# Optimization experiments

Measured on AMD Instinct MI355X. Metric: run time of the kernel, lower is better.

## Reference

```python
import jax, jax.numpy as jnp
import numpy as np

B, N, NODE_DIM = 8, 128, 64
L, RES_DIM = 512, 1024
CG, CP = 128, 128
NUM_GNN_STEPS = 3
HID = CG + CP // 2  # interaction hidden = 192


def setup_inputs() -> dict:
    key = jax.random.key(0)
    ks = jax.random.split(key, 20)
    a = (jax.random.uniform(ks[0], (B, N, N)) < 0.05).astype(jnp.float32)
    adj = jnp.clip(a + jnp.swapaxes(a, 1, 2), 0.0, 1.0)
    adj = adj * (1.0 - jnp.eye(N, dtype=jnp.float32))
    nodes = jax.random.normal(ks[1], (B, N, NODE_DIM), dtype=jnp.float32)
    prot = jax.random.normal(ks[2], (B, L, RES_DIM), dtype=jnp.float32)
    s = 0.02
    inp = {
        "adj_mats": adj, "nodes": nodes, "protein_sequences": prot,
        "Wn": jax.random.normal(ks[3], (NODE_DIM, CG)) * s, "bn": jnp.zeros((CG,)),
        "Wg": jax.random.normal(ks[4], (CG, CG)) * s, "bg": jnp.zeros((CG,)),
        "Wr": jax.random.normal(ks[5], (RES_DIM, CP)) * s, "br": jnp.zeros((CP,)),
        "Wa": jax.random.normal(ks[6], (CG + CP, 1)) * s, "ba": jnp.zeros((1,)),
        "W1": jax.random.normal(ks[7], (CG + CP, HID)) * s, "b1": jnp.zeros((HID,)),
        "W2": jax.random.normal(ks[8], (HID, CG)) * s, "b2": jnp.zeros((CG,)),
        "Wo": jax.random.normal(ks[9], (CG, 1)) * s, "bo": jnp.zeros((1,)),
    }
    return inp


def reference(adj_mats, nodes, protein_sequences,
              Wn, bn, Wg, bg, Wr, br, Wa, ba, W1, b1, W2, b2, Wo, bo):
    # node compression: [B,N,CG]
    h = nodes @ Wn + bn
    deg = jnp.clip(jnp.sum(adj_mats, axis=-1), 1.0, None)        # [B,N]
    norm = deg ** -0.5                                           # [B,N]
    for i in range(NUM_GNN_STEPS):
        m = jnp.einsum('bij,bjc->bic', adj_mats, h * norm[..., None])
        h = (m * norm[..., None]) @ Wg + bg
        h = jnp.tanh(h) if i == NUM_GNN_STEPS - 1 else jax.nn.relu(h)
    # residue compression: [B,L,CP]
    r = protein_sequences @ Wr + br
    # MergeSnE1: all-pairs broadcast concat -> [B, N*L, CG+CP]
    cat = jnp.concatenate([
        jnp.broadcast_to(h[:, :, None, :], (B, N, L, CG)),
        jnp.broadcast_to(r[:, None, :, :], (B, N, L, CP)),
    ], axis=-1).reshape(B, N * L, CG + CP)
    # attention: Linear -> Softmax over last dim (size 1 => all ones, faithful)
    attn = jax.nn.softmax(cat @ Wa + ba, axis=-1)                # [B,N*L,1]
    inter = jax.nn.relu(cat @ W1 + b1) @ W2 + b2                 # [B,N*L,CG]
    weighted_sum = jnp.sum(attn * inter, axis=1)                 # [B,CG]
    return weighted_sum @ Wo + bo                                # [B,1]
```

## Files before the change

### kernel.cpp

```cpp
#include <hip/hip_runtime.h>

#define BB 8
#define NN 128
#define ND 64
#define LL 512
#define RD 1024
#define CG 128
#define HID 192

typedef __attribute__((ext_vector_type(8))) short short8;
typedef __attribute__((ext_vector_type(4))) float f32x4;

__device__ __forceinline__ unsigned short f2bf(float x) {
    unsigned u = __builtin_bit_cast(unsigned, x);
    u += 0x7fffu + ((u >> 16) & 1u);
    return (unsigned short)(u >> 16);
}
__device__ __forceinline__ float bf2f(unsigned short h) {
    unsigned u = ((unsigned)h) << 16;
    return __builtin_bit_cast(float, u);
}
#define MFMA __builtin_amdgcn_mfma_f32_16x16x32_bf16

__global__ __launch_bounds__(512, 1) void k_prep(
    const float* __restrict__ adj, const float* __restrict__ nodes,
    const float* __restrict__ Wn, const float* __restrict__ bn,
    const float* __restrict__ Wr, const float* __restrict__ br,
    const float* __restrict__ W1, const float* __restrict__ b1,
    const float* __restrict__ Wg, const float* __restrict__ bg,
    const float* __restrict__ W2, const float* __restrict__ b2,
    const float* __restrict__ Wo, const float* __restrict__ bo,
    unsigned short* __restrict__ WcT, unsigned short* __restrict__ hW1b,
    float* __restrict__ vbuf, float* __restrict__ out)
{
    __shared__ unsigned short hT[NN][136];
    __shared__ unsigned short mbuf[NN][72];
    __shared__ unsigned short WgT[NN][136];
    __shared__ unsigned short W1T[HID][136];
    __shared__ float snorm[NN];
    __shared__ float b1cL[HID];
    __shared__ float sbg[NN];
    int t = threadIdx.x, blk = blockIdx.x;
    int w = t >> 6, l = t & 63, lr = l & 15, ks = l >> 4, lk = ks * 8;
    const float* W1b = W1 + CG * HID;

    if (blk < 16) {
        int r0 = blk * 64;
        #pragma unroll
        for (int q = 0; q < 48; ++q) {
            int e = t + 512 * q;
            int m = e / HID, c = e % HID;
            W1T[c][m] = f2bf(W1[(size_t)(CG + m) * HID + c]);
        }
        int rt = w & 3, jh = w >> 2;
        short8 awr[4];
        #pragma unroll
        for (int kk = 0; kk < 4; ++kk) {
            const float* wp = Wr + (size_t)(r0 + rt * 16 + lr) * CG + kk * 32 + lk;
            float4 q0 = *(const float4*)wp;
            float4 q1 = *(const float4*)(wp + 4);
            unsigned short u[8];
            u[0]=f2bf(q0.x); u[1]=f2bf(q0.y); u[2]=f2bf(q0.z); u[3]=f2bf(q0.w);
            u[4]=f2bf(q1.x); u[5]=f2bf(q1.y); u[6]=f2bf(q1.z); u[7]=f2bf(q1.w);
            awr[kk] = *(const short8*)u;
        }
        __syncthreads();
        #pragma unroll
        for (int jt6 = 0; jt6 < 6; ++jt6) {
            int jt = jh * 6 + jt6;
            f32x4 d = {0.f, 0.f, 0.f, 0.f};
            #pragma unroll
            for (int kk = 0; kk < 4; ++kk) {
                short8 bf = *(const short8*)(&W1T[jt * 16 + lr][kk * 32 + lk]);
                d = MFMA(awr[kk], bf, d, 0, 0, 0);
            }
            unsigned short u[4];
            #pragma unroll
            for (int i = 0; i < 4; ++i) u[i] = f2bf(d[i]);
            *(uint2*)(WcT + (size_t)(jt * 16 + lr) * RD + r0 + rt * 16 + ks * 4) = *(uint2*)u;
        }
        return;
    }
    if (blk == 16) {
        if (t < HID) {
            float s = 0.f;
            #pragma unroll 8
            for (int k = 0; k < CG; ++k) s = fmaf(W2[t * CG + k], Wo[k], s);
            vbuf[t] = s;
        }
        if (t < BB) {
            float s = 0.f;
            for (int k = 0; k < CG; ++k) s = fmaf(b2[k], Wo[k], s);
            out[t] = (float)(NN * LL) * s + bo[0];
        }
        return;
    }

    int b = blk - 17;
    int i0 = w * 16;

    {
        float* dscr = (float*)&mbuf[0][0];
        int row = t >> 2, q4 = t & 3;
        const float* ar = adj + ((size_t)b * NN + row) * NN + q4 * 32;
        float d = 0.f;
        #pragma unroll
        for (int c4 = 0; c4 < 8; ++c4) {
            float4 p = *(const float4*)(ar + c4 * 4);
            d += (p.x + p.y) + (p.z + p.w);
        }
        dscr[row * 4 + q4] = d;
        __syncthreads();
        if (t < NN) {
            snorm[t] = rsqrtf(fmaxf(dscr[t*4] + dscr[t*4+1] + dscr[t*4+2] + dscr[t*4+3], 1.f));
        } else if (t < 320) {
            int j = t - 128;
            float s = b1[j];
            #pragma unroll 8
            for (int m = 0; m < CG; ++m)
                s = fmaf(br[m], W1b[(size_t)m * HID + j], s);
            b1cL[j] = s;
        } else if (t < 448) {
            sbg[t - 320] = bg[t - 320];
        }
        __syncthreads();
    }

    unsigned short* WnT = &mbuf[0][0];
    #pragma unroll
    for (int q = 0; q < 16; ++q) {
        int e = t + 512 * q;
        int c = e & 127, k = e >> 7;
        WnT[c * 72 + k] = f2bf(Wn[(size_t)k * CG + c]);
    }
    #pragma unroll
    for (int q = 0; q < 32; ++q) {
        int e = t + 512 * q;
        int c = e & 127, j = e >> 7;
        WgT[c][j] = f2bf(Wg[(size_t)j * CG + c]);
    }
    #pragma unroll
    for (int q = 0; q < 32; ++q) {
        int e = t + 512 * q;
        int jj = e & 127, k = e >> 7;
        W1T[jj][k] = f2bf(W1[(size_t)k * HID + jj]);
    }
    #pragma unroll
    for (int q = 0; q < 16; ++q) {
        int e = t + 512 * q;
        int jj = 128 + (e & 63), k = e >> 6;
        W1T[jj][k] = f2bf(W1[(size_t)k * HID + jj]);
    }

    short8 af[4];
    {
        float ni = snorm[i0 + lr];
        const float* ar = adj + ((size_t)b * NN + i0 + lr) * NN;
        #pragma unroll
        for (int kk = 0; kk < 4; ++kk) {
            int kb = kk * 32 + lk;
            float4 p0 = *(const float4*)(ar + kb);
            float4 p1 = *(const float4*)(ar + kb + 4);
            unsigned short u[8];
            u[0] = f2bf(p0.x * ni * snorm[kb+0]); u[1] = f2bf(p0.y * ni * snorm[kb+1]);
            u[2] = f2bf(p0.z * ni * snorm[kb+2]); u[3] = f2bf(p0.w * ni * snorm[kb+3]);
            u[4] = f2bf(p1.x * ni * snorm[kb+4]); u[5] = f2bf(p1.y * ni * snorm[kb+5]);
            u[6] = f2bf(p1.z * ni * snorm[kb+6]); u[7] = f2bf(p1.w * ni * snorm[kb+7]);
            af[kk] = *(const short8*)u;
        }
    }
    short8 bnod[2];
    #pragma unroll
    for (int kk = 0; kk < 2; ++kk) {
        const float* np = nodes + ((size_t)b * NN + i0 + lr) * ND + kk * 32 + lk;
        float4 q0 = *(const float4*)np;
        float4 q1 = *(const float4*)(np + 4);
        unsigned short u[8];
        u[0]=f2bf(q0.x); u[1]=f2bf(q0.y); u[2]=f2bf(q0.z); u[3]=f2bf(q0.w);
        u[4]=f2bf(q1.x); u[5]=f2bf(q1.y); u[6]=f2bf(q1.z); u[7]=f2bf(q1.w);
        bnod[kk] = *(const short8*)u;
    }
    __syncthreads();

    #pragma unroll
    for (int ct = 0; ct < 8; ++ct) {
        f32x4 d = {0.f, 0.f, 0.f, 0.f};
        #pragma unroll
        for (int kk = 0; kk < 2; ++kk) {
            short8 afw = *(const short8*)(WnT + (ct * 16 + lr) * 72 + kk * 32 + lk);
            d = MFMA(afw, bnod[kk], d, 0, 0, 0);
        }
        #pragma unroll
        for (int i = 0; i < 4; ++i)
            hT[ct * 16 + ks * 4 + i][i0 + lr] = f2bf(d[i] + bn[ct * 16 + ks * 4 + i]);
    }
    __syncthreads();

    for (int s = 0; s < 3; ++s) {
        f32x4 acc8[8];
        #pragma unroll
        for (int ct = 0; ct < 8; ++ct) acc8[ct] = (f32x4){0.f, 0.f, 0.f, 0.f};
        #pragma unroll
        for (int hf = 0; hf < 2; ++hf) {
            #pragma unroll
            for (int jt = 0; jt < 4; ++jt) {
                int jg = hf * 64 + jt * 16;
                f32x4 d = {0.f, 0.f, 0.f, 0.f};
                #pragma unroll
                for (int kk = 0; kk < 4; ++kk) {
                    short8 bf = *(const short8*)(&hT[jg + lr][kk * 32 + lk]);
                    d = MFMA(af[kk], bf, d, 0, 0, 0);
                }
                #pragma unroll
                for (int i = 0; i < 4; ++i)
                    mbuf[i0 + ks * 4 + i][jt * 16 + lr] = f2bf(d[i]);
            }
            short8 bm[2];
            #pragma unroll
            for (int kk = 0; kk < 2; ++kk)
                bm[kk] = *(const short8*)(&mbuf[i0 + lr][kk * 32 + lk]);
            #pragma unroll
            for (int ct = 0; ct < 8; ++ct) {
                #pragma unroll
                for (int kk = 0; kk < 2; ++kk) {
                    short8 wf = *(const short8*)(&WgT[ct * 16 + lr][hf * 64 + kk * 32 + lk]);
                    if (s < 2)
                        acc8[ct] = MFMA(wf, bm[kk], acc8[ct], 0, 0, 0);
                    else
                        acc8[ct] = MFMA(bm[kk], wf, acc8[ct], 0, 0, 0);
                }
            }
        }
        __syncthreads();
        if (s < 2) {
            #pragma unroll
            for (int ct = 0; ct < 8; ++ct)
                #pragma unroll
                for (int i = 0; i < 4; ++i)
                    hT[ct * 16 + ks * 4 + i][i0 + lr] =
                        f2bf(fmaxf(acc8[ct][i] + sbg[ct * 16 + ks * 4 + i], 0.f));
        } else {
            #pragma unroll
            for (int ct = 0; ct < 8; ++ct)
                #pragma unroll
                for (int i = 0; i < 4; ++i)
                    hT[i0 + ks * 4 + i][ct * 16 + lr] =
                        f2bf(tanhf(acc8[ct][i] + sbg[ct * 16 + lr]));
        }
        __syncthreads();
    }

    {
        short8 bh[4];
        #pragma unroll
        for (int kk = 0; kk < 4; ++kk)
            bh[kk] = *(const short8*)(&hT[i0 + lr][kk * 32 + lk]);
        #pragma unroll
        for (int jjt = 0; jjt < 12; ++jjt) {
            f32x4 d = {0.f, 0.f, 0.f, 0.f};
            #pragma unroll
            for (int kk = 0; kk < 4; ++kk) {
                short8 wf = *(const short8*)(&W1T[jjt * 16 + lr][kk * 32 + lk]);
                d = MFMA(wf, bh[kk], d, 0, 0, 0);
            }
            #pragma unroll
            for (int i = 0; i < 4; ++i) {
                int jj = jjt * 16 + ks * 4 + i;
                hW1b[(size_t)b * HID * NN + jj * NN + i0 + lr] = f2bf(d[i] + b1cL[jj]);
            }
        }
    }
}

__global__ __launch_bounds__(512, 1) void k_gemm(
    const float* __restrict__ prot, const unsigned short* __restrict__ WcT,
    const unsigned short* __restrict__ hW1b, const float* __restrict__ vbuf,
    float* __restrict__ out)
{
    __shared__ unsigned short aT[16 * 1032];
    __shared__ unsigned short h1[HID * 136];
    __shared__ float pbuf[2 * 16 * 192];
    __shared__ float sred[8];
    int t = threadIdx.x, blk = blockIdx.x;
    int b = blk >> 5, lc = blk & 31;
    int w = t >> 6, l = t & 63, lr = l & 15, ks = l >> 4, lk = ks * 8;
    int w2 = w >> 2, wj = w & 3;

    #pragma unroll
    for (int q = 0; q < 4; ++q) {
        int e = t + 512 * q;
        int row = e >> 7;
        int c8 = (e & 127) * 8;
        const float* pr = prot + ((size_t)(b * LL + lc * 16 + row)) * RD + c8;
        float4 p0 = *(const float4*)pr;
        float4 p1 = *(const float4*)(pr + 4);
        unsigned short u[8];
        u[0]=f2bf(p0.x); u[1]=f2bf(p0.y); u[2]=f2bf(p0.z); u[3]=f2bf(p0.w);
        u[4]=f2bf(p1.x); u[5]=f2bf(p1.y); u[6]=f2bf(p1.z); u[7]=f2bf(p1.w);
        *(short8*)(aT + row * 1032 + c8) = *(const short8*)u;
    }
    #pragma unroll
    for (int q = 0; q < 6; ++q) {
        int u8 = t + 512 * q;
        int row = u8 >> 4;
        int n8 = (u8 & 15) * 8;
        short8 v = *(const short8*)(hW1b + (size_t)b * HID * NN + row * NN + n8);
        *(short8*)(h1 + row * 136 + n8) = v;
    }
    float v0 = vbuf[wj * 48 + lr];
    float v1 = vbuf[wj * 48 + 16 + lr];
    float v2 = vbuf[wj * 48 + 32 + lr];
    __syncthreads();

    f32x4 a0 = {0.f,0.f,0.f,0.f}, a1 = a0, a2 = a0;
    {
        const unsigned short* ap = aT + lr * 1032 + w2 * 512 + lk;
        const unsigned short* bp = WcT + (size_t)(wj * 48 + lr) * RD + w2 * 512 + lk;
        #pragma unroll 4
        for (int k0 = 0; k0 < 512; k0 += 32) {
            short8 av = *(const short8*)(ap + k0);
            short8 b0 = *(const short8*)(bp + k0);
            short8 b1 = *(const short8*)(bp + 16 * RD + k0);
            short8 b2 = *(const short8*)(bp + 32 * RD + k0);
            a0 = MFMA(av, b0, a0, 0, 0, 0);
            a1 = MFMA(av, b1, a1, 0, 0, 0);
            a2 = MFMA(av, b2, a2, 0, 0, 0);
        }
    }
    #pragma unroll
    for (int i = 0; i < 4; ++i) {
        int r = ks * 4 + i;
        pbuf[(w2 * 16 + r) * 192 + wj * 48 + lr]      = a0[i];
        pbuf[(w2 * 16 + r) * 192 + wj * 48 + 16 + lr] = a1[i];
        pbuf[(w2 * 16 + r) * 192 + wj * 48 + 32 + lr] = a2[i];
    }
    __syncthreads();
    float rw0[4], rw1[4], rw2[4];
    #pragma unroll
    for (int i = 0; i < 4; ++i) {
        int r = ks * 4 + i;
        rw0[i] = pbuf[r * 192 + wj*48 + lr]      + pbuf[(16 + r) * 192 + wj*48 + lr];
        rw1[i] = pbuf[r * 192 + wj*48 + 16 + lr] + pbuf[(16 + r) * 192 + wj*48 + 16 + lr];
        rw2[i] = pbuf[r * 192 + wj*48 + 32 + lr] + pbuf[(16 + r) * 192 + wj*48 + 32 + lr];
    }

    const unsigned short* h0p = h1 + (wj * 48 + lr) * 136 + w2 * 64;
    const unsigned short* h1p = h0p + 16 * 136;
    const unsigned short* h2p = h0p + 32 * 136;
    float s = 0.f;
    #pragma unroll 2
    for (int n0 = 0; n0 < 64; n0 += 4) {
        unsigned short e0[4], e1[4], e2[4];
        *(uint2*)e0 = *(const uint2*)(h0p + n0);
        *(uint2*)e1 = *(const uint2*)(h1p + n0);
        *(uint2*)e2 = *(const uint2*)(h2p + n0);
        #pragma unroll
        for (int q = 0; q < 4; ++q) {
            float hh0 = bf2f(e0[q]), hh1 = bf2f(e1[q]), hh2 = bf2f(e2[q]);
            #pragma unroll
            for (int i = 0; i < 4; ++i) {
                s = fmaf(v0, fmaxf(rw0[i] + hh0, 0.f), s);
                s = fmaf(v1, fmaxf(rw1[i] + hh1, 0.f), s);
                s = fmaf(v2, fmaxf(rw2[i] + hh2, 0.f), s);
            }
        }
    }
    for (int off = 32; off; off >>= 1) s += __shfl_down(s, off);
    if (l == 0) sred[w] = s;
    __syncthreads();
    if (t == 0) {
        float tot = ((sred[0] + sred[1]) + (sred[2] + sred[3]))
                  + ((sred[4] + sred[5]) + (sred[6] + sred[7]));
        atomicAdd(&out[b], tot);
    }
}

extern "C" void kernel_launch(void* const* d_in, const int* in_sizes, int n_in,
                              void* d_out, int out_size, void* d_ws, size_t ws_size,
                              hipStream_t stream)
{
    const float* adj   = (const float*)d_in[0];
    const float* nodes = (const float*)d_in[1];
    const float* prot  = (const float*)d_in[2];
    const float* Wn    = (const float*)d_in[3];
    const float* bn    = (const float*)d_in[4];
    const float* Wg    = (const float*)d_in[5];
    const float* bg    = (const float*)d_in[6];
    const float* Wr    = (const float*)d_in[7];
    const float* br    = (const float*)d_in[8];
    const float* W1    = (const float*)d_in[11];
    const float* b1    = (const float*)d_in[12];
    const float* W2    = (const float*)d_in[13];
    const float* b2    = (const float*)d_in[14];
    const float* Wo    = (const float*)d_in[15];
    const float* bo    = (const float*)d_in[16];

    float* ws     = (float*)d_ws;
    float* vbuf   = ws;
    unsigned short* hW1b = (unsigned short*)(ws + 192);
    unsigned short* WcT  = hW1b + (size_t)BB * HID * NN;
    float* out    = (float*)d_out;

    hipLaunchKernelGGL(k_prep, dim3(25), dim3(512), 0, stream,
                       adj, nodes, Wn, bn, Wr, br, W1, b1, Wg, bg,
                       W2, b2, Wo, bo, WcT, hW1b, vbuf, out);
    hipLaunchKernelGGL(k_gemm, dim3(256), dim3(512), 0, stream,
                       prot, WcT, hW1b, vbuf, out);
}
```

Measured before the change: 55.18 us.

## Vectorize weight transposes, drop h1 LDS staging, split accumulators, raise occupancy

Weight transposes in k_prep now use float4 global loads, each spread over four LDS stores, where before every element needed its own scalar load. k_gemm stops staging hW1b into shared memory and reads it straight from global memory (L2-resident). This frees about 52KB of LDS, and launch bounds are raised to 4 blocks per CU. The epilogue reduction uses four independent accumulators to break the serial FMA dependency chain. Direct global reads in the inner loop may add latency, and the higher launch bound may cap the register count.

Measured after the change: 63.40 us. 1.15x slower.

```diff
diff --git a/kernel.cpp b/kernel.cpp
--- a/kernel.cpp
+++ b/kernel.cpp
@@ -47,10 +47,14 @@
     if (blk < 16) {
         int r0 = blk * 64;
         #pragma unroll
-        for (int q = 0; q < 48; ++q) {
-            int e = t + 512 * q;
-            int m = e / HID, c = e % HID;
-            W1T[c][m] = f2bf(W1[(size_t)(CG + m) * HID + c]);
+        for (int q = 0; q < 12; ++q) {
+            int e4 = t + 512 * q;
+            int m = e4 / 48, c = (e4 % 48) * 4;
+            float4 v = *(const float4*)(W1 + (size_t)(CG + m) * HID + c);
+            W1T[c][m]     = f2bf(v.x);
+            W1T[c + 1][m] = f2bf(v.y);
+            W1T[c + 2][m] = f2bf(v.z);
+            W1T[c + 3][m] = f2bf(v.w);
         }
         int rt = w & 3, jh = w >> 2;
         short8 awr[4];
@@ -128,28 +132,34 @@
 
     unsigned short* WnT = &mbuf[0][0];
     #pragma unroll
-    for (int q = 0; q < 16; ++q) {
-        int e = t + 512 * q;
-        int c = e & 127, k = e >> 7;
-        WnT[c * 72 + k] = f2bf(Wn[(size_t)k * CG + c]);
-    }
-    #pragma unroll
-    for (int q = 0; q < 32; ++q) {
-        int e = t + 512 * q;
-        int c = e & 127, j = e >> 7;
-        WgT[c][j] = f2bf(Wg[(size_t)j * CG + c]);
-    }
-    #pragma unroll
-    for (int q = 0; q < 32; ++q) {
-        int e = t + 512 * q;
-        int jj = e & 127, k = e >> 7;
-        W1T[jj][k] = f2bf(W1[(size_t)k * HID + jj]);
-    }
-    #pragma unroll
-    for (int q = 0; q < 16; ++q) {
-        int e = t + 512 * q;
-        int jj = 128 + (e & 63), k = e >> 6;
-        W1T[jj][k] = f2bf(W1[(size_t)k * HID + jj]);
+    for (int q = 0; q < 4; ++q) {
+        int e4 = t + 512 * q;
+        int k = e4 >> 5, c = (e4 & 31) * 4;
+        float4 v = *(const float4*)(Wn + (size_t)k * CG + c);
+        WnT[c * 72 + k]       = f2bf(v.x);
+        WnT[(c + 1) * 72 + k] = f2bf(v.y);
+        WnT[(c + 2) * 72 + k] = f2bf(v.z);
+        WnT[(c + 3) * 72 + k] = f2bf(v.w);
+    }
+    #pragma unroll
+    for (int q = 0; q < 8; ++q) {
+        int e4 = t + 512 * q;
+        int j = e4 >> 5, c = (e4 & 31) * 4;
+        float4 v = *(const float4*)(Wg + (size_t)j * CG + c);
+        WgT[c][j]     = f2bf(v.x);
+        WgT[c + 1][j] = f2bf(v.y);
+        WgT[c + 2][j] = f2bf(v.z);
+        WgT[c + 3][j] = f2bf(v.w);
+    }
+    #pragma unroll
+    for (int q = 0; q < 12; ++q) {
+        int e4 = t + 512 * q;
+        int k = e4 / 48, jj = (e4 % 48) * 4;
+        float4 v = *(const float4*)(W1 + (size_t)k * HID + jj);
+        W1T[jj][k]     = f2bf(v.x);
+        W1T[jj + 1][k] = f2bf(v.y);
+        W1T[jj + 2][k] = f2bf(v.z);
+        W1T[jj + 3][k] = f2bf(v.w);
     }
 
     short8 af[4];
@@ -272,13 +282,12 @@
     }
 }
 
-__global__ __launch_bounds__(512, 1) void k_gemm(
+__global__ __launch_bounds__(512, 4) void k_gemm(
     const float* __restrict__ prot, const unsigned short* __restrict__ WcT,
     const unsigned short* __restrict__ hW1b, const float* __restrict__ vbuf,
     float* __restrict__ out)
 {
     __shared__ unsigned short aT[16 * 1032];
-    __shared__ unsigned short h1[HID * 136];
     __shared__ float pbuf[2 * 16 * 192];
     __shared__ float sred[8];
     int t = threadIdx.x, blk = blockIdx.x;
@@ -298,14 +307,6 @@
         u[0]=f2bf(p0.x); u[1]=f2bf(p0.y); u[2]=f2bf(p0.z); u[3]=f2bf(p0.w);
         u[4]=f2bf(p1.x); u[5]=f2bf(p1.y); u[6]=f2bf(p1.z); u[7]=f2bf(p1.w);
         *(short8*)(aT + row * 1032 + c8) = *(const short8*)u;
-    }
-    #pragma unroll
-    for (int q = 0; q < 6; ++q) {
-        int u8 = t + 512 * q;
-        int row = u8 >> 4;
-        int n8 = (u8 & 15) * 8;
-        short8 v = *(const short8*)(hW1b + (size_t)b * HID * NN + row * NN + n8);
-        *(short8*)(h1 + row * 136 + n8) = v;
     }
     float v0 = vbuf[wj * 48 + lr];
     float v1 = vbuf[wj * 48 + 16 + lr];
@@ -344,11 +345,12 @@
         rw2[i] = pbuf[r * 192 + wj*48 + 32 + lr] + pbuf[(16 + r) * 192 + wj*48 + 32 + lr];
     }
 
-    const unsigned short* h0p = h1 + (wj * 48 + lr) * 136 + w2 * 64;
-    const unsigned short* h1p = h0p + 16 * 136;
-    const unsigned short* h2p = h0p + 32 * 136;
-    float s = 0.f;
-    #pragma unroll 2
+    const unsigned short* hb = hW1b + (size_t)b * HID * NN;
+    const unsigned short* h0p = hb + (size_t)(wj * 48 + lr) * NN + w2 * 64;
+    const unsigned short* h1p = h0p + 16 * NN;
+    const unsigned short* h2p = h0p + 32 * NN;
+    float s0 = 0.f, s1 = 0.f, s2 = 0.f, s3 = 0.f;
+    #pragma unroll 4
     for (int n0 = 0; n0 < 64; n0 += 4) {
         unsigned short e0[4], e1[4], e2[4];
         *(uint2*)e0 = *(const uint2*)(h0p + n0);
@@ -357,14 +359,18 @@
         #pragma unroll
         for (int q = 0; q < 4; ++q) {
             float hh0 = bf2f(e0[q]), hh1 = bf2f(e1[q]), hh2 = bf2f(e2[q]);
+            float* sq = (q == 0) ? &s0 : (q == 1) ? &s1 : (q == 2) ? &s2 : &s3;
+            float sl = *sq;
             #pragma unroll
             for (int i = 0; i < 4; ++i) {
-                s = fmaf(v0, fmaxf(rw0[i] + hh0, 0.f), s);
-                s = fmaf(v1, fmaxf(rw1[i] + hh1, 0.f), s);
-                s = fmaf(v2, fmaxf(rw2[i] + hh2, 0.f), s);
-            }
-        }
-    }
+                sl = fmaf(v0, fmaxf(rw0[i] + hh0, 0.f), sl);
+                sl = fmaf(v1, fmaxf(rw1[i] + hh1, 0.f), sl);
+                sl = fmaf(v2, fmaxf(rw2[i] + hh2, 0.f), sl);
+            }
+            *sq = sl;
+        }
+    }
+    float s = (s0 + s1) + (s2 + s3);
     for (int off = 32; off; off >>= 1) s += __shfl_down(s, off);
     if (l == 0) sred[w] = s;
     __syncthreads();
```
